# Kernel optimization log

Hardware: AMD Instinct MI355X
Metric: run time of the kernel (lower is better)

Reference implementation:

```python
import jax, jax.numpy as jnp
import numpy as np

B, NN, NC, H, V, K = 1024, 16, 16, 64, 100, 8
C = NN + NC
NEG = -1e9


def _ln_all(x, eps=1e-5):
    # torch.layer_norm(x, x.shape): normalize over ALL elements, no affine
    mu = x.mean()
    var = ((x - mu) ** 2).mean()
    return (x - mu) * jax.lax.rsqrt(var + eps)


def _ln_last(x, g, b, eps=1e-5):
    # nn.LayerNorm(H) with affine params
    mu = x.mean(-1, keepdims=True)
    var = ((x - mu) ** 2).mean(-1, keepdims=True)
    return (x - mu) * jax.lax.rsqrt(var + eps) * g + b


def _masked_ln(x, m, eps=1e-5):
    # x: [C,B,H], m: [C,B]; full-tensor layernorm over in-graph nodes only
    cnt = jnp.maximum(m.sum(1) * x.shape[-1], 1.0)
    mu = (x * m[..., None]).sum((1, 2)) / cnt
    d = x - mu[:, None, None]
    var = ((d * d) * m[..., None]).sum((1, 2)) / cnt
    return d * jax.lax.rsqrt(var + eps)[:, None, None]


def _forward(num_data, cat_data, num_w, num_b, cat_emb, fi_w1, fi_b1, fi_g, fi_be,
             fi_w2, fi_b2, gcn1_w, gcn1_b, gcn2_w, gcn2_b, pw1, pb1, pg, pbe, pw2, pb2):
    # numeric columns: Linear(1,H) per column == scalar * w + b
    fe_num = num_data[..., None] * num_w[None] + num_b[None]              # [B,NN,H]
    fe_num = _ln_all(jax.nn.relu(fe_num.reshape(B, NN * H)))
    fe_cat = cat_emb[jnp.arange(NC)[None, :], cat_data]                   # [B,NC,H]
    fe_cat = _ln_all(fe_cat.reshape(B, NC * H))
    feat = jnp.concatenate([fe_num, fe_cat], axis=1)                      # [B,C*H]
    fe3 = feat.reshape(B, C, H)
    # shared feature-importance MLP applied to every column slice (dropout = eval)
    h = _ln_last(jax.nn.relu(fe3 @ fi_w1 + fi_b1), fi_g, fi_be)
    imp = _ln_all((h @ fi_w2 + fi_b2)[..., 0])                            # [B,C]
    fe3 = fe3 * imp[..., None]
    feat = fe3.reshape(B, C * H)
    # top-K column selection per row + masked softmax
    _, idx = jax.lax.top_k(imp, K)                                        # [B,K]
    mask = jnp.zeros((B, C), jnp.float32).at[jnp.arange(B)[:, None], idx].set(1.0)
    p = jax.nn.softmax(jnp.where(mask > 0, imp, NEG), axis=1) * mask      # [B,C]
    # graph c: nodes = rows with column c in their top-K; zero column c,
    # adjacency = P P^T with zero diagonal, softmax over nonzero entries
    mT = mask.T                                                           # [C,B]
    pm = p[None, :, :] * mT[:, :, None] * (1.0 - jnp.eye(C))[:, None, :]  # [C,B,C]
    S = jnp.einsum('cik,cjk->cij', pm, pm)                                # [C,B,B]
    S = S * (1.0 - jnp.eye(B))
    pos = S > 0
    mx = jnp.max(jnp.where(pos, S, -jnp.inf), axis=(1, 2))
    mx = jnp.where(jnp.isfinite(mx), mx, 0.0)
    E = jnp.where(pos, jnp.exp(S - mx[:, None, None]), 0.0)
    Z = E.sum((1, 2))
    w = E / jnp.where(Z > 0, Z, 1.0)[:, None, None]
    # GCNConv normalization: add self-loops (weight 1) for in-graph nodes
    A = w + jnp.eye(B)[None] * mT[:, :, None]
    deg = A.sum(-1)
    dinv = jnp.where(deg > 0, jax.lax.rsqrt(deg), 0.0)
    An = dinv[:, :, None] * A * dinv[:, None, :]                          # [C,B,B]
    x = jnp.einsum('cij,jh->cih', An, feat @ gcn1_w) + gcn1_b
    x = _masked_ln(jax.nn.relu(x), mT)
    x = jnp.einsum('cij,cjh->cih', An, x @ gcn2_w) + gcn2_b
    x = _masked_ln(jax.nn.relu(x), mT)                                    # [C,B,H]
    # reassembly: each row gathers its K graph outputs, ordered by column id
    cols = jnp.sort(idx, axis=1)                                          # [B,K]
    gathered = x[cols, jnp.arange(B)[:, None]]                            # [B,K,H]
    full = jnp.concatenate([gathered, fe3], axis=1).reshape(B, (K + C) * H)
    return _ln_last(jax.nn.relu(full @ pw1 + pb1), pg, pbe) @ pw2 + pb2   # [B,2]


def setup_inputs() -> dict:
    key = jax.random.key(0)
    ks = jax.random.split(key, 12)
    s = 0.05
    f = jnp.float32
    return {
        'num_data': jax.random.normal(ks[0], (B, NN), f),
        'cat_data': jax.random.randint(ks[1], (B, NC), 0, V, jnp.int32),
        'num_w': jax.random.normal(ks[2], (NN, H), f) * s,
        'num_b': jnp.zeros((NN, H), f),
        'cat_emb': jax.random.normal(ks[3], (NC, V, H), f) * s,
        'fi_w1': jax.random.normal(ks[4], (H, H), f) * s,
        'fi_b1': jnp.zeros((H,), f),
        'fi_g': jnp.ones((H,), f),
        'fi_be': jnp.zeros((H,), f),
        'fi_w2': jax.random.normal(ks[5], (H, 1), f) * s,
        'fi_b2': jnp.zeros((1,), f),
        'gcn1_w': jax.random.normal(ks[6], (C * H, H), f) * s,
        'gcn1_b': jnp.zeros((H,), f),
        'gcn2_w': jax.random.normal(ks[7], (H, H), f) * s,
        'gcn2_b': jnp.zeros((H,), f),
        'pw1': jax.random.normal(ks[8], ((K + C) * H, H), f) * s,
        'pb1': jnp.zeros((H,), f),
        'pg': jnp.ones((H,), f),
        'pbe': jnp.zeros((H,), f),
        'pw2': jax.random.normal(ks[9], (H, 2), f) * s,
        'pb2': jnp.zeros((2,), f),
    }


def reference(num_data, cat_data, num_w, num_b, cat_emb, fi_w1, fi_b1, fi_g, fi_be,
              fi_w2, fi_b2, gcn1_w, gcn1_b, gcn2_w, gcn2_b, pw1, pb1, pg, pbe, pw2, pb2):
    return _forward(num_data, cat_data, num_w, num_b, cat_emb, fi_w1, fi_b1, fi_g, fi_be,
                    fi_w2, fi_b2, gcn1_w, gcn1_b, gcn2_w, gcn2_b, pw1, pb1, pg, pbe, pw2, pb2)
```

## Files before the change

kernel.cpp:

```cpp
#include <hip/hip_runtime.h>
#include <hip/hip_bf16.h>

#define BB   1024
#define NNUM 16
#define NCAT 16
#define HH   64
#define VV   100
#define KK   8
#define CC   32
#define CH   2048
#define FULLW 2560

#define OFF_FE3   0u
#define OFF_X1    2097152u
#define OFF_X2    4194304u
#define OFF_G     6291456u
#define OFF_SIMP  6356992u
#define OFF_P     6389760u
#define OFF_ROWE  6422528u
#define OFF_DINV  6455296u
#define OFF_F     6488064u
#define OFF_STATS 6520832u
#define OFF_Z     6520840u
#define OFF_X1S   6520872u
#define OFF_X2S   6520936u
#define OFF_COLS  6521000u
#define OFF_LIST  6529192u
#define OFF_CNT   6561960u
#define OFF_AOFF  6561992u
#define OFF_AN    6562048u

__device__ inline float wsum64(float v){
  #pragma unroll
  for (int o = 32; o; o >>= 1) v += __shfl_xor(v, o);
  return v;
}

__global__ __launch_bounds__(256) void k_init(float* ws){
  int t = threadIdx.x;
  if (t < 8)  ws[OFF_STATS + t] = 0.f;
  if (t < 64) ws[OFF_X1S + t] = 0.f;
  if (t < 64) ws[OFF_X2S + t] = 0.f;
  if (t < 32) ws[OFF_Z + t] = 0.f;
}

__global__ __launch_bounds__(256) void k_fe(const float* __restrict__ nd,
                                            const float* __restrict__ nw,
                                            const float* __restrict__ nb,
                                            const int* __restrict__ cd,
                                            const float* __restrict__ emb,
                                            float* __restrict__ ws){
  float* fe3 = ws + OFF_FE3;
  float lsn = 0.f, lssn = 0.f, lsc = 0.f, lssc = 0.f;
  int idx = blockIdx.x*256 + threadIdx.x;
  {
    int h4 = idx & 15, fn = (idx >> 4) & 15, b = (idx >> 8) & 1023;
    bool isNum = (idx < 262144);
    if (isNum){
      float s = nd[b*NNUM + fn];
      float4 w = *(const float4*)&nw[fn*HH + h4*4];
      float4 bi = *(const float4*)&nb[fn*HH + h4*4];
      float4 v;
      v.x = fmaxf(s*w.x + bi.x, 0.f);
      v.y = fmaxf(s*w.y + bi.y, 0.f);
      v.z = fmaxf(s*w.z + bi.z, 0.f);
      v.w = fmaxf(s*w.w + bi.w, 0.f);
      *(float4*)&fe3[b*CH + fn*HH + h4*4] = v;
      lsn = v.x+v.y+v.z+v.w;
      lssn = v.x*v.x+v.y*v.y+v.z*v.z+v.w*v.w;
    } else {
      int j = cd[b*NCAT + fn];
      float4 v = *(const float4*)&emb[((size_t)fn*VV + j)*HH + h4*4];
      *(float4*)&fe3[b*CH + (NNUM + fn)*HH + h4*4] = v;
      lsc = v.x+v.y+v.z+v.w;
      lssc = v.x*v.x+v.y*v.y+v.z*v.z+v.w*v.w;
    }
  }
  __shared__ float sh[16];
  lsn = wsum64(lsn); lssn = wsum64(lssn);
  lsc = wsum64(lsc); lssc = wsum64(lssc);
  int w = threadIdx.x >> 6;
  if ((threadIdx.x & 63) == 0){ sh[w] = lsn; sh[4+w] = lssn; sh[8+w] = lsc; sh[12+w] = lssc; }
  __syncthreads();
  if (threadIdx.x == 0){
    if (blockIdx.x < 1024){
      atomicAdd(ws + OFF_STATS + 0, sh[0]+sh[1]+sh[2]+sh[3]);
      atomicAdd(ws + OFF_STATS + 1, sh[4]+sh[5]+sh[6]+sh[7]);
    } else {
      atomicAdd(ws + OFF_STATS + 2, sh[8]+sh[9]+sh[10]+sh[11]);
      atomicAdd(ws + OFF_STATS + 3, sh[12]+sh[13]+sh[14]+sh[15]);
    }
  }
}

__global__ __launch_bounds__(256) void k_normfe(float* __restrict__ ws){
  const float Ninv = 1.f/1048576.f;
  int idx4 = blockIdx.x*256 + threadIdx.x;
  float* fe3 = ws + OFF_FE3;
  const float* st = ws + OFF_STATS;
  int c = (idx4 & 511) >> 4;
  float s, ssq;
  if (c < NNUM){ s = st[0]; ssq = st[1]; } else { s = st[2]; ssq = st[3]; }
  float mu = s*Ninv;
  float var = ssq*Ninv - mu*mu;
  float rs = rsqrtf(var + 1e-5f);
  float4 v = *(float4*)&fe3[idx4*4];
  v.x = (v.x - mu)*rs; v.y = (v.y - mu)*rs; v.z = (v.z - mu)*rs; v.w = (v.w - mu)*rs;
  *(float4*)&fe3[idx4*4] = v;
}

__global__ __launch_bounds__(256) void k_fi(const float* __restrict__ w1,
                                            const float* __restrict__ b1,
                                            const float* __restrict__ g,
                                            const float* __restrict__ be,
                                            const float* __restrict__ w2,
                                            const float* __restrict__ b2f,
                                            float* __restrict__ ws){
  __shared__ float w1s[64][65];
  __shared__ float xs[4][64];
  int wv = threadIdx.x >> 6, lane = threadIdx.x & 63;
  for (int q = threadIdx.x; q < 4096; q += 256) w1s[q >> 6][q & 63] = w1[q];
  __syncthreads();
  const float* fe3 = ws + OFF_FE3;
  float b1l = b1[lane], gl = g[lane], bel = be[lane], w2l = w2[lane], b2s = b2f[0];
  int gw = blockIdx.x*4 + wv;
  float ls = 0.f, lss = 0.f;
  for (int it = 0; it < 8; ++it){
    int row = gw + 4096*it;
    float x = fe3[(size_t)row*64 + lane];
    xs[wv][lane] = x;
    float t0 = 0.f, t1 = 0.f, t2 = 0.f, t3 = 0.f;
    #pragma unroll
    for (int k = 0; k < 64; k += 4){
      float4 xq = *(const float4*)&xs[wv][k];
      t0 += xq.x*w1s[k][lane];
      t1 += xq.y*w1s[k+1][lane];
      t2 += xq.z*w1s[k+2][lane];
      t3 += xq.w*w1s[k+3][lane];
    }
    float t = (t0+t1) + (t2+t3) + b1l;
    t = fmaxf(t, 0.f);
    float mu = wsum64(t)*(1.f/64.f);
    float d = t - mu;
    float var = wsum64(d*d)*(1.f/64.f);
    float rs = rsqrtf(var + 1e-5f);
    float h1 = d*rs*gl + bel;
    float s = wsum64(h1*w2l) + b2s;
    if (lane == 0) ws[OFF_SIMP + row] = s;
    ls += s; lss += s*s;
  }
  __shared__ float sh[8];
  if (lane == 0){ sh[wv] = ls; sh[4+wv] = lss; }
  __syncthreads();
  if (threadIdx.x == 0){
    atomicAdd(ws + OFF_STATS + 4, sh[0]+sh[1]+sh[2]+sh[3]);
    atomicAdd(ws + OFF_STATS + 5, sh[4]+sh[5]+sh[6]+sh[7]);
  }
}

__global__ __launch_bounds__(256) void k_topk(float* __restrict__ ws){
  int b = blockIdx.x;
  __shared__ float imp[CC];
  if (threadIdx.x < CC){
    const float Ninv = 1.f/32768.f;
    float s4 = ws[OFF_STATS+4], s5 = ws[OFF_STATS+5];
    float mu = s4*Ninv, var = s5*Ninv - mu*mu;
    float rs = rsqrtf(var + 1e-5f);
    imp[threadIdx.x] = (ws[OFF_SIMP + b*CC + threadIdx.x] - mu)*rs;
  }
  __syncthreads();
  if (threadIdx.x == 0){
    unsigned taken = 0;
    float m0 = 0.f;
    for (int t = 0; t < KK; t++){
      float best = -1e30f; int bi = 0;
      for (int c = 0; c < CC; c++){
        if (!((taken >> c) & 1u) && imp[c] > best){ best = imp[c]; bi = c; }
      }
      taken |= 1u << bi;
      if (t == 0) m0 = best;
    }
    float sum = 0.f;
    int* cols = (int*)(ws + OFF_COLS);
    int tn = 0;
    for (int c = 0; c < CC; c++){
      if ((taken >> c) & 1u){ cols[b*KK + tn] = c; tn++; sum += expf(imp[c] - m0); }
    }
    float inv = 1.f/sum;
    for (int c = 0; c < CC; c++){
      float pv = ((taken >> c) & 1u) ? expf(imp[c] - m0)*inv : 0.f;
      ws[OFF_P + b*CC + c] = pv;
    }
  }
  __syncthreads();
  float* fe3 = ws + OFF_FE3;
  for (int kq = threadIdx.x; kq < CH; kq += 256){
    fe3[b*CH + kq] *= imp[kq >> 6];
  }
}

__global__ __launch_bounds__(256) void k_lists(float* __restrict__ ws){
  int c = blockIdx.x;
  __shared__ int cnt_s;
  if (threadIdx.x == 0) cnt_s = 0;
  __syncthreads();
  int* list = (int*)(ws + OFF_LIST);
  for (int b = threadIdx.x; b < BB; b += 256){
    if (ws[OFF_P + b*CC + c] > 0.f){
      int slot = atomicAdd(&cnt_s, 1);
      list[c*BB + slot] = b;
    }
  }
  __syncthreads();
  if (threadIdx.x == 0) ((int*)(ws + OFF_CNT))[c] = cnt_s;
}

__global__ void k_offs(float* __restrict__ ws){
  if (threadIdx.x == 0){
    const int* cnt = (const int*)(ws + OFF_CNT);
    int* aoff = (int*)(ws + OFF_AOFF);
    int acc = 0;
    for (int c = 0; c < CC; c++){ aoff[c] = acc; acc += cnt[c]*cnt[c]; }
    aoff[CC] = acc;
  }
}

__global__ __launch_bounds__(256) void k_G(const float* __restrict__ w1g, float* __restrict__ ws){
  __shared__ float frow[4][CH];
  int wv = threadIdx.x >> 6, lane = threadIdx.x & 63;
  int b = blockIdx.x*4 + wv;
  const float* fe3 = ws + OFF_FE3;
  for (int q = 0; q < 32; q++) frow[wv][q*64 + lane] = fe3[b*CH + q*64 + lane];
  __syncthreads();
  float a0 = 0.f, a1 = 0.f, a2 = 0.f, a3 = 0.f;
  #pragma unroll 8
  for (int k = 0; k < CH; k += 4){
    float4 fq = *(const float4*)&frow[wv][k];
    a0 += fq.x*w1g[(k+0)*64 + lane];
    a1 += fq.y*w1g[(k+1)*64 + lane];
    a2 += fq.z*w1g[(k+2)*64 + lane];
    a3 += fq.w*w1g[(k+3)*64 + lane];
  }
  ws[OFF_G + b*64 + lane] = (a0+a1) + (a2+a3);
}

__global__ __launch_bounds__(256) void k_E(float* __restrict__ ws){
  int c = blockIdx.x;
  int n = ((const int*)(ws + OFF_CNT))[c];
  int r0 = blockIdx.y*32;
  if (r0 >= n) return;
  const int* list = (const int*)(ws + OFF_LIST) + c*BB;
  const float* p = ws + OFF_P;
  int base = ((const int*)(ws + OFF_AOFF))[c];
  float* An = ws + OFF_AN;
  __shared__ float pis[32][36];
  __shared__ float pT[32][72];
  int wv = threadIdx.x >> 6, lane = threadIdx.x & 63;
  for (int idx = threadIdx.x; idx < 1024; idx += 256){
    int r = idx >> 5, u = idx & 31;
    int ii = r0 + r;
    float v = 0.f;
    if (ii < n && u != c) v = p[list[ii]*CC + u];
    pis[r][u] = v;
  }
  float re[8] = {0.f,0.f,0.f,0.f,0.f,0.f,0.f,0.f};
  int rowBase = r0 + wv*8;
  for (int jt = 0; jt < n; jt += 64){
    __syncthreads();
    for (int idx = threadIdx.x; idx < 2048; idx += 256){
      int t = idx & 63, u = idx >> 6;
      int jj = jt + t;
      float v = 0.f;
      if (jj < n) v = p[list[jj]*CC + u];
      pT[u][t] = v;
    }
    __syncthreads();
    int jj = jt + lane;
    bool jok = (jj < n);
    #pragma unroll
    for (int r = 0; r < 8; r++){
      int row = rowBase + r;
      if (row < n){
        float4 pi0 = *(const float4*)&pis[wv*8 + r][0];
        float4 pi1 = *(const float4*)&pis[wv*8 + r][4];
        float4 pi2 = *(const float4*)&pis[wv*8 + r][8];
        float4 pi3 = *(const float4*)&pis[wv*8 + r][12];
        float4 pi4 = *(const float4*)&pis[wv*8 + r][16];
        float4 pi5 = *(const float4*)&pis[wv*8 + r][20];
        float4 pi6 = *(const float4*)&pis[wv*8 + r][24];
        float4 pi7 = *(const float4*)&pis[wv*8 + r][28];
        float s0 = pi0.x*pT[0][lane]  + pi1.x*pT[4][lane]  + pi2.x*pT[8][lane]  + pi3.x*pT[12][lane]
                 + pi4.x*pT[16][lane] + pi5.x*pT[20][lane] + pi6.x*pT[24][lane] + pi7.x*pT[28][lane];
        float s1 = pi0.y*pT[1][lane]  + pi1.y*pT[5][lane]  + pi2.y*pT[9][lane]  + pi3.y*pT[13][lane]
                 + pi4.y*pT[17][lane] + pi5.y*pT[21][lane] + pi6.y*pT[25][lane] + pi7.y*pT[29][lane];
        float s2 = pi0.z*pT[2][lane]  + pi1.z*pT[6][lane]  + pi2.z*pT[10][lane] + pi3.z*pT[14][lane]
                 + pi4.z*pT[18][lane] + pi5.z*pT[22][lane] + pi6.z*pT[26][lane] + pi7.z*pT[30][lane];
        float s3 = pi0.w*pT[3][lane]  + pi1.w*pT[7][lane]  + pi2.w*pT[11][lane] + pi3.w*pT[15][lane]
                 + pi4.w*pT[19][lane] + pi5.w*pT[23][lane] + pi6.w*pT[27][lane] + pi7.w*pT[31][lane];
        float S = (s0+s1) + (s2+s3);
        float Ev = 0.f;
        if (jok && jj != row && S > 0.f) Ev = __expf(S);
        if (jok) An[(size_t)base + (size_t)row*n + jj] = Ev;
        re[r] += Ev;
      }
    }
  }
  float zpart = 0.f;
  #pragma unroll
  for (int r = 0; r < 8; r++){
    float rsum = wsum64(re[r]);
    int row = rowBase + r;
    if (lane == 0 && row < n){
      ws[OFF_ROWE + c*BB + row] = rsum;
      zpart += rsum;
    }
  }
  __shared__ float sh[4];
  if (lane == 0) sh[wv] = zpart;
  __syncthreads();
  if (threadIdx.x == 0) atomicAdd(ws + OFF_Z + c, sh[0]+sh[1]+sh[2]+sh[3]);
}

__global__ __launch_bounds__(256) void k_scl(float* __restrict__ ws){
  int c = blockIdx.x;
  int n = ((const int*)(ws + OFF_CNT))[c];
  int ii = blockIdx.y*256 + threadIdx.x;
  if (ii >= n) return;
  float z = ws[OFF_Z + c];
  float zp = (z > 0.f) ? z : 1.f;
  float re = ws[OFF_ROWE + c*BB + ii];
  float di = rsqrtf(re/zp + 1.0f);
  ws[OFF_DINV + c*BB + ii] = di;
  ws[OFF_F    + c*BB + ii] = di*rsqrtf(zp);
}

__global__ __launch_bounds__(256) void k_agg(const float* __restrict__ src, int chanStride,
                                             const float* __restrict__ bias,
                                             float* __restrict__ outb,
                                             float* __restrict__ statsb,
                                             float* __restrict__ ws){
  int c = blockIdx.x;
  int n = ((const int*)(ws + OFF_CNT))[c];
  int r0 = blockIdx.y*32;
  if (r0 >= n) return;
  int base = ((const int*)(ws + OFF_AOFF))[c];
  const int* lst = (const int*)(ws + OFF_LIST) + c*BB;
  const float* E = ws + OFF_AN + (size_t)base;
  const float* fpos = ws + OFF_F + c*BB;
  const float* dpos = ws + OFF_DINV + c*BB;
  const float* srcc = src + (size_t)c*(size_t)chanStride*64;
  __shared__ float cf[32][128];
  __shared__ int   ls[128];
  __shared__ float frow_s[32];
  int wv = threadIdx.x >> 6, lane = threadIdx.x & 63;
  if (threadIdx.x < 32){
    int rr = r0 + threadIdx.x;
    frow_s[threadIdx.x] = (rr < n) ? fpos[rr] : 0.f;
  }
  int rw = wv*8;
  float acc[8] = {0.f,0.f,0.f,0.f,0.f,0.f,0.f,0.f};
  for (int jt = 0; jt < n; jt += 128){
    __syncthreads();
    if (threadIdx.x < 128){
      int jj = jt + threadIdx.x;
      ls[threadIdx.x] = (jj < n) ? lst[jj] : 0;
    }
    for (int idx = threadIdx.x; idx < 4096; idx += 256){
      int r = idx >> 7, j = idx & 127;
      int row = r0 + r, jj = jt + j;
      float v = 0.f;
      if (row < n && jj < n){
        if (jj == row){ float d = dpos[row]; v = d*d; }
        else v = E[(size_t)row*n + jj] * fpos[jj] * frow_s[r];
      }
      cf[r][j] = v;
    }
    __syncthreads();
    int jcnt = n - jt; if (jcnt > 128) jcnt = 128;
    int jcnt4 = (jcnt + 3) & ~3;
    for (int j = 0; j < jcnt4; j += 4){
      float v0 = srcc[(size_t)ls[j+0]*64 + lane];
      float v1 = srcc[(size_t)ls[j+1]*64 + lane];
      float v2 = srcc[(size_t)ls[j+2]*64 + lane];
      float v3 = srcc[(size_t)ls[j+3]*64 + lane];
      #pragma unroll
      for (int r = 0; r < 8; r++){
        float4 c4 = *(const float4*)&cf[rw + r][j];
        acc[r] += c4.x*v0 + c4.y*v1 + c4.z*v2 + c4.w*v3;
      }
    }
  }
  float bl = bias[lane];
  float s = 0.f, ssq = 0.f;
  #pragma unroll
  for (int r = 0; r < 8; r++){
    int row = r0 + rw + r;
    if (row < n){
      float a = fmaxf(acc[r] + bl, 0.f);
      outb[((size_t)c*BB + lst[row])*64 + lane] = a;
      s += a; ssq += a*a;
    }
  }
  s = wsum64(s); ssq = wsum64(ssq);
  __shared__ float shs[4], shq[4];
  if (lane == 0){ shs[wv] = s; shq[wv] = ssq; }
  __syncthreads();
  if (threadIdx.x == 0){
    float ts = shs[0]+shs[1]+shs[2]+shs[3];
    float tq = shq[0]+shq[1]+shq[2]+shq[3];
    if (tq != 0.f){
      atomicAdd(statsb + 2*c,     ts);
      atomicAdd(statsb + 2*c + 1, tq);
    }
  }
}

__global__ __launch_bounds__(256) void k_y(const float* __restrict__ w2g, float* __restrict__ ws){
  __shared__ float w2s[64][65];
  __shared__ float xs[4][64];
  int wv = threadIdx.x >> 6, lane = threadIdx.x & 63;
  for (int q = threadIdx.x; q < 4096; q += 256) w2s[q >> 6][q & 63] = w2g[q];
  __syncthreads();
  int c = blockIdx.x;
  int n = ((const int*)(ws + OFF_CNT))[c];
  const int* list = (const int*)(ws + OFF_LIST);
  float* x1 = ws + OFF_X1;
  float cntf = fmaxf((float)(n*64), 1.f);
  float mu = ws[OFF_X1S + 2*c]/cntf;
  float var = ws[OFF_X1S + 2*c + 1]/cntf - mu*mu;
  float rs = rsqrtf(var + 1e-5f);
  for (int ii = blockIdx.y*4 + wv; ii < n; ii += 64){
    int i = list[c*BB + ii];
    size_t bse = ((size_t)c*BB + i)*64;
    float xn = (x1[bse + lane] - mu)*rs;
    xs[wv][lane] = xn;
    float y0 = 0.f, y1 = 0.f, y2 = 0.f, y3 = 0.f;
    #pragma unroll
    for (int k = 0; k < 64; k += 4){
      float4 xq = *(const float4*)&xs[wv][k];
      y0 += xq.x*w2s[k][lane];
      y1 += xq.y*w2s[k+1][lane];
      y2 += xq.z*w2s[k+2][lane];
      y3 += xq.w*w2s[k+3][lane];
    }
    x1[bse + lane] = (y0+y1) + (y2+y3);
  }
}

__global__ __launch_bounds__(256) void k_final(const float* __restrict__ pw1,
                                               const float* __restrict__ pb1,
                                               const float* __restrict__ pg,
                                               const float* __restrict__ pbe,
                                               const float* __restrict__ pw2,
                                               const float* __restrict__ pb2,
                                               float* __restrict__ ws,
                                               float* __restrict__ out){
  __shared__ float fr[4][FULLW];
  int wv = threadIdx.x >> 6, lane = threadIdx.x & 63;
  int b = blockIdx.x*4 + wv;
  const int* cols = (const int*)(ws + OFF_COLS);
  const int* cnt  = (const int*)(ws + OFF_CNT);
  const float* x2 = ws + OFF_X2;
  const float* fe3 = ws + OFF_FE3;
  #pragma unroll
  for (int t = 0; t < KK; t++){
    int ct = cols[b*KK + t];
    float cf = fmaxf((float)(cnt[ct]*64), 1.f);
    float mu = ws[OFF_X2S + 2*ct]/cf;
    float var = ws[OFF_X2S + 2*ct + 1]/cf - mu*mu;
    float rs = rsqrtf(var + 1e-5f);
    fr[wv][t*64 + lane] = (x2[((size_t)ct*BB + b)*64 + lane] - mu)*rs;
  }
  #pragma unroll
  for (int q = 0; q < 32; q++) fr[wv][512 + q*64 + lane] = fe3[b*CH + q*64 + lane];
  __syncthreads();
  float a0 = 0.f, a1 = 0.f, a2 = 0.f, a3 = 0.f;
  #pragma unroll 8
  for (int k = 0; k < FULLW; k += 4){
    float4 fq = *(const float4*)&fr[wv][k];
    a0 += fq.x*pw1[(k+0)*64 + lane];
    a1 += fq.y*pw1[(k+1)*64 + lane];
    a2 += fq.z*pw1[(k+2)*64 + lane];
    a3 += fq.w*pw1[(k+3)*64 + lane];
  }
  float acc = (a0+a1) + (a2+a3) + pb1[lane];
  acc = fmaxf(acc, 0.f);
  float mu = wsum64(acc)*(1.f/64.f);
  float d = acc - mu;
  float var = wsum64(d*d)*(1.f/64.f);
  float rs = rsqrtf(var + 1e-5f);
  float zn = d*rs*pg[lane] + pbe[lane];
  float s0 = wsum64(zn*pw2[lane*2 + 0]);
  float s1 = wsum64(zn*pw2[lane*2 + 1]);
  if (lane == 0){
    out[b*2 + 0] = s0 + pb2[0];
    out[b*2 + 1] = s1 + pb2[1];
  }
}

extern "C" void kernel_launch(void* const* d_in, const int* in_sizes, int n_in,
                              void* d_out, int out_size, void* d_ws, size_t ws_size,
                              hipStream_t stream){
  (void)in_sizes; (void)n_in; (void)out_size; (void)ws_size;
  const float* num_data = (const float*)d_in[0];
  const int*   cat_data = (const int*)d_in[1];
  const float* num_w   = (const float*)d_in[2];
  const float* num_b   = (const float*)d_in[3];
  const float* cat_emb = (const float*)d_in[4];
  const float* fi_w1   = (const float*)d_in[5];
  const float* fi_b1   = (const float*)d_in[6];
  const float* fi_g    = (const float*)d_in[7];
  const float* fi_be   = (const float*)d_in[8];
  const float* fi_w2   = (const float*)d_in[9];
  const float* fi_b2   = (const float*)d_in[10];
  const float* gcn1_w  = (const float*)d_in[11];
  const float* gcn1_b  = (const float*)d_in[12];
  const float* gcn2_w  = (const float*)d_in[13];
  const float* gcn2_b  = (const float*)d_in[14];
  const float* pw1     = (const float*)d_in[15];
  const float* pb1     = (const float*)d_in[16];
  const float* pg      = (const float*)d_in[17];
  const float* pbe     = (const float*)d_in[18];
  const float* pw2     = (const float*)d_in[19];
  const float* pb2     = (const float*)d_in[20];
  float* ws  = (float*)d_ws;
  float* out = (float*)d_out;

  k_init<<<1, 256, 0, stream>>>(ws);
  k_fe<<<2048, 256, 0, stream>>>(num_data, num_w, num_b, cat_data, cat_emb, ws);
  k_normfe<<<2048, 256, 0, stream>>>(ws);
  k_fi<<<1024, 256, 0, stream>>>(fi_w1, fi_b1, fi_g, fi_be, fi_w2, fi_b2, ws);
  k_topk<<<1024, 256, 0, stream>>>(ws);
  k_lists<<<32, 256, 0, stream>>>(ws);
  k_offs<<<1, 64, 0, stream>>>(ws);
  k_G<<<256, 256, 0, stream>>>(gcn1_w, ws);
  k_E<<<dim3(32, 32), 256, 0, stream>>>(ws);
  k_scl<<<dim3(32, 4), 256, 0, stream>>>(ws);
  k_agg<<<dim3(32, 32), 256, 0, stream>>>(ws + OFF_G, 0, gcn1_b, ws + OFF_X1, ws + OFF_X1S, ws);
  k_y<<<dim3(32, 16), 256, 0, stream>>>(gcn2_w, ws);
  k_agg<<<dim3(32, 32), 256, 0, stream>>>(ws + OFF_X1, BB, gcn2_b, ws + OFF_X2, ws + OFF_X2S, ws);
  k_final<<<256, 256, 0, stream>>>(pw1, pb1, pg, pbe, pw2, pb2, ws, out);
}
```

Measured before the change: 538.8 us.

## Stage gathered source rows in shared memory and halve k_agg row tile

k_agg now cooperatively gathers the 128 neighbour feature rows of each j-tile into shared memory with float4 loads, instead of every wave reloading them from global memory through the index list. The row tile per block shrinks from 32 to 16, so there are twice as many blocks in y. The goal is to cut redundant scattered global reads and raise parallelism, since each row was previously read by all four waves. The cost is about 40KB of shared memory per block, which may limit occupancy, and each gathered row is now reused by fewer output rows per block.

```diff
diff --git a/kernel.cpp b/kernel.cpp
--- a/kernel.cpp
+++ b/kernel.cpp
@@ -341,7 +341,7 @@
                                              float* __restrict__ ws){
   int c = blockIdx.x;
   int n = ((const int*)(ws + OFF_CNT))[c];
-  int r0 = blockIdx.y*32;
+  int r0 = blockIdx.y*16;
   if (r0 >= n) return;
   int base = ((const int*)(ws + OFF_AOFF))[c];
   const int* lst = (const int*)(ws + OFF_LIST) + c*BB;
@@ -349,23 +349,33 @@
   const float* fpos = ws + OFF_F + c*BB;
   const float* dpos = ws + OFF_DINV + c*BB;
   const float* srcc = src + (size_t)c*(size_t)chanStride*64;
-  __shared__ float cf[32][128];
-  __shared__ int   ls[128];
-  __shared__ float frow_s[32];
+  __shared__ float cf[16][128];
+  __shared__ float sl[128][64];
+  __shared__ float frow_s[16];
   int wv = threadIdx.x >> 6, lane = threadIdx.x & 63;
-  if (threadIdx.x < 32){
+  if (threadIdx.x < 16){
     int rr = r0 + threadIdx.x;
     frow_s[threadIdx.x] = (rr < n) ? fpos[rr] : 0.f;
   }
-  int rw = wv*8;
-  float acc[8] = {0.f,0.f,0.f,0.f,0.f,0.f,0.f,0.f};
+  int rw = wv*4;
+  float acc[4] = {0.f,0.f,0.f,0.f};
   for (int jt = 0; jt < n; jt += 128){
     __syncthreads();
-    if (threadIdx.x < 128){
-      int jj = jt + threadIdx.x;
-      ls[threadIdx.x] = (jj < n) ? lst[jj] : 0;
-    }
-    for (int idx = threadIdx.x; idx < 4096; idx += 256){
+    #pragma unroll
+    for (int s = 0; s < 8; s++){
+      int slot = threadIdx.x + s*256;
+      int j = slot >> 4, q = slot & 15;
+      int jj = jt + j;
+      float4 v = make_float4(0.f,0.f,0.f,0.f);
+      if (jj < n){
+        int jg = lst[jj];
+        v = *(const float4*)&srcc[(size_t)jg*64 + q*4];
+      }
+      *(float4*)&sl[j][q*4] = v;
+    }
+    #pragma unroll
+    for (int s = 0; s < 8; s++){
+      int idx = threadIdx.x + s*256;
       int r = idx >> 7, j = idx & 127;
       int row = r0 + r, jj = jt + j;
       float v = 0.f;
@@ -379,12 +389,12 @@
     int jcnt = n - jt; if (jcnt > 128) jcnt = 128;
     int jcnt4 = (jcnt + 3) & ~3;
     for (int j = 0; j < jcnt4; j += 4){
-      float v0 = srcc[(size_t)ls[j+0]*64 + lane];
-      float v1 = srcc[(size_t)ls[j+1]*64 + lane];
-      float v2 = srcc[(size_t)ls[j+2]*64 + lane];
-      float v3 = srcc[(size_t)ls[j+3]*64 + lane];
+      float v0 = sl[j+0][lane];
+      float v1 = sl[j+1][lane];
+      float v2 = sl[j+2][lane];
+      float v3 = sl[j+3][lane];
       #pragma unroll
-      for (int r = 0; r < 8; r++){
+      for (int r = 0; r < 4; r++){
         float4 c4 = *(const float4*)&cf[rw + r][j];
         acc[r] += c4.x*v0 + c4.y*v1 + c4.z*v2 + c4.w*v3;
       }
@@ -393,7 +403,7 @@
   float bl = bias[lane];
   float s = 0.f, ssq = 0.f;
   #pragma unroll
-  for (int r = 0; r < 8; r++){
+  for (int r = 0; r < 4; r++){
     int row = r0 + rw + r;
     if (row < n){
       float a = fmaxf(acc[r] + bl, 0.f);
@@ -536,8 +546,8 @@
   k_G<<<256, 256, 0, stream>>>(gcn1_w, ws);
   k_E<<<dim3(32, 32), 256, 0, stream>>>(ws);
   k_scl<<<dim3(32, 4), 256, 0, stream>>>(ws);
-  k_agg<<<dim3(32, 32), 256, 0, stream>>>(ws + OFF_G, 0, gcn1_b, ws + OFF_X1, ws + OFF_X1S, ws);
+  k_agg<<<dim3(32, 64), 256, 0, stream>>>(ws + OFF_G, 0, gcn1_b, ws + OFF_X1, ws + OFF_X1S, ws);
   k_y<<<dim3(32, 16), 256, 0, stream>>>(gcn2_w, ws);
-  k_agg<<<dim3(32, 32), 256, 0, stream>>>(ws + OFF_X1, BB, gcn2_b, ws + OFF_X2, ws + OFF_X2S, ws);
+  k_agg<<<dim3(32, 64), 256, 0, stream>>>(ws + OFF_X1, BB, gcn2_b, ws + OFF_X2, ws + OFF_X2S, ws);
   k_final<<<256, 256, 0, stream>>>(pw1, pb1, pg, pbe, pw2, pb2, ws, out);
 }
```

Measured after the change: 535.2 us. Within noise of the previous version (-0.7%).
